# Optimization experiments

Measured on AMD Instinct MI355X. Metric: run time of the kernel, lower is better.

## Reference

```python
import jax, jax.numpy as jnp
import numpy as np

B, S, D, H = 2, 2048, 1024, 16
DK = D // H

def setup_inputs() -> dict:
    key = jax.random.key(0)
    ks = jax.random.split(key, 8)
    inp = {
        "Q": jax.random.normal(ks[0], (B, S, D), dtype=jnp.float32),
        "K": jax.random.normal(ks[1], (B, S, D), dtype=jnp.float32),
        "V": jax.random.normal(ks[2], (B, S, D), dtype=jnp.float32),
        "mask": jax.random.randint(ks[3], (B, 1, S, S), 0, 2, dtype=jnp.int32),
        # nn.Linear weights, shape [out_features, in_features], no bias
        "Wq": jax.random.normal(ks[4], (D, D), dtype=jnp.float32) / np.sqrt(D),
        "Wk": jax.random.normal(ks[5], (D, D), dtype=jnp.float32) / np.sqrt(D),
        "Wv": jax.random.normal(ks[6], (D, D), dtype=jnp.float32) / np.sqrt(D),
        "Wo": jax.random.normal(ks[7], (D, D), dtype=jnp.float32) / np.sqrt(D),
    }
    return inp

def reference(Q, K, V, mask, Wq, Wk, Wv, Wo):
    b, s, d = Q.shape
    # projections: y = x @ W.T (torch nn.Linear convention)
    q = (Q @ Wq.T).reshape(b, s, H, DK).transpose(0, 2, 1, 3)  # [b,h,s,dk]
    k = (K @ Wk.T).reshape(b, -1, H, DK).transpose(0, 2, 1, 3)
    v = (V @ Wv.T).reshape(b, -1, H, DK).transpose(0, 2, 1, 3)
    score = jnp.einsum("bhqd,bhkd->bhqk", q, k) / jnp.sqrt(jnp.float32(DK))
    # faithful to source: masked positions get value 1e-9 BEFORE softmax
    score = jnp.where(mask == 0, jnp.float32(1e-9), score)
    attn = jax.nn.softmax(score, axis=-1)
    # dropout p=0.1 treated as eval-mode identity
    out = jnp.einsum("bhqk,bhkd->bhqd", attn, v)  # [b,h,s,dk]
    out = out.transpose(0, 2, 1, 3).reshape(b, s, d)
    return out @ Wo.T
```

## Files before the change

### kernel.cpp

```cpp
#include <hip/hip_runtime.h>

typedef unsigned short u16;
typedef __attribute__((ext_vector_type(8))) short bf16x8;
typedef __attribute__((ext_vector_type(4))) float f32x4;

constexpr int B_  = 2;
constexpr int S_  = 2048;
constexpr int D_  = 1024;
constexpr int H_  = 16;
constexpr int DK_ = 64;
constexpr int NROW = B_ * S_;
constexpr size_t QSZ = (size_t)B_ * H_ * S_ * DK_;

__device__ __forceinline__ u16 f2bf(float f) {
    union { float f; unsigned u; } c; c.f = f;
    unsigned r = c.u + 0x7fffu + ((c.u >> 16) & 1u);
    return (u16)(r >> 16);
}
__device__ __forceinline__ unsigned pack2(float a, float b) {
    return (unsigned)f2bf(a) | ((unsigned)f2bf(b) << 16);
}

constexpr int GP = 40;

__global__ __launch_bounds__(256, 3)
void qkv_mfma(const float* __restrict__ Xq, const float* __restrict__ Xk,
              const float* __restrict__ Xv,
              const float* __restrict__ Wq, const float* __restrict__ Wk,
              const float* __restrict__ Wv,
              u16* __restrict__ Yq, u16* __restrict__ Yk, u16* __restrict__ Yv)
{
    __shared__ u16 As[128][GP];
    __shared__ u16 Bs[128][GP];

    const int z = blockIdx.z;
    const float* X = (z == 0) ? Xq : (z == 1) ? Xk : Xv;
    const float* W = (z == 0) ? Wq : (z == 1) ? Wk : Wv;
    u16*         Y = (z == 0) ? Yq : (z == 1) ? Yk : Yv;
    const float osc = (z == 0) ? 0.125f : 1.0f;

    const int tid  = threadIdx.x;
    const int lane = tid & 63;
    const int w    = tid >> 6;
    const int quad = lane >> 4;
    const int lq   = lane & 15;
    const int wm   = (w & 1) << 6;
    const int wn   = (w >> 1) << 6;

    const int m0 = blockIdx.x << 7;
    const int n0 = blockIdx.y << 7;

    const int srow = tid >> 1;
    const int skh  = (tid & 1) << 4;

    const float* xrow = X + (size_t)(m0 + srow) * D_ + skh;
    const float* wrow = W + (size_t)(n0 + srow) * D_ + skh;

    f32x4 acc[4][4];
#pragma unroll
    for (int i = 0; i < 4; ++i)
#pragma unroll
        for (int j = 0; j < 4; ++j) acc[i][j] = (f32x4){0.f, 0.f, 0.f, 0.f};

    float4 xa[4], wa[4];
#pragma unroll
    for (int u = 0; u < 4; ++u) {
        xa[u] = *(const float4*)(xrow + (u << 2));
        wa[u] = *(const float4*)(wrow + (u << 2));
    }

    for (int it = 0; it < D_ / 32; ++it) {
        __syncthreads();
        {
            uint4 px, pw;
            px.x = pack2(xa[0].x, xa[0].y); px.y = pack2(xa[0].z, xa[0].w);
            px.z = pack2(xa[1].x, xa[1].y); px.w = pack2(xa[1].z, xa[1].w);
            *(uint4*)&As[srow][skh] = px;
            px.x = pack2(xa[2].x, xa[2].y); px.y = pack2(xa[2].z, xa[2].w);
            px.z = pack2(xa[3].x, xa[3].y); px.w = pack2(xa[3].z, xa[3].w);
            *(uint4*)&As[srow][skh + 8] = px;
            pw.x = pack2(wa[0].x, wa[0].y); pw.y = pack2(wa[0].z, wa[0].w);
            pw.z = pack2(wa[1].x, wa[1].y); pw.w = pack2(wa[1].z, wa[1].w);
            *(uint4*)&Bs[srow][skh] = pw;
            pw.x = pack2(wa[2].x, wa[2].y); pw.y = pack2(wa[2].z, wa[2].w);
            pw.z = pack2(wa[3].x, wa[3].y); pw.w = pack2(wa[3].z, wa[3].w);
            *(uint4*)&Bs[srow][skh + 8] = pw;
        }
        __syncthreads();

        if (it + 1 < D_ / 32) {
            const int kk = (it + 1) << 5;
#pragma unroll
            for (int u = 0; u < 4; ++u) {
                xa[u] = *(const float4*)(xrow + kk + (u << 2));
                wa[u] = *(const float4*)(wrow + kk + (u << 2));
            }
        }

        bf16x8 af[4], bf[4];
#pragma unroll
        for (int t = 0; t < 4; ++t) {
            af[t] = *(const bf16x8*)&As[wm + (t << 4) + lq][quad << 3];
            bf[t] = *(const bf16x8*)&Bs[wn + (t << 4) + lq][quad << 3];
        }
#pragma unroll
        for (int i = 0; i < 4; ++i)
#pragma unroll
            for (int j = 0; j < 4; ++j)
                acc[i][j] = __builtin_amdgcn_mfma_f32_16x16x32_bf16(
                    af[i], bf[j], acc[i][j], 0, 0, 0);
    }

#pragma unroll
    for (int i = 0; i < 4; ++i)
#pragma unroll
        for (int j = 0; j < 4; ++j)
#pragma unroll
            for (int r = 0; r < 4; ++r) {
                const int grow = m0 + wm + (i << 4) + (quad << 2) + r;
                const int of   = n0 + wn + (j << 4) + lq;
                const int b = grow >> 11, s = grow & (S_ - 1);
                const int h = of >> 6,    dk = of & 63;
                Y[(((size_t)(b * H_ + h)) * S_ + s) * DK_ + dk] =
                    f2bf(acc[i][j][r] * osc);
            }
}

__global__ __launch_bounds__(256, 2)
void outproj_mfma(const u16* __restrict__ X, const float* __restrict__ W,
                  float* __restrict__ Y)
{
    __shared__ u16 As[64][GP];
    __shared__ u16 Bs[128][GP];

    const int tid  = threadIdx.x;
    const int lane = tid & 63;
    const int w    = tid >> 6;
    const int quad = lane >> 4;
    const int lq   = lane & 15;
    const int wn   = w << 5;

    const int m0 = blockIdx.x << 6;
    const int n0 = blockIdx.y << 7;

    const int ar = tid >> 2;
    const int ac = (tid & 3) << 3;
    const int br = tid >> 1;
    const int bc = (tid & 1) << 4;

    const u16*   xrow = X + (size_t)(m0 + ar) * D_ + ac;
    const float* wrow = W + (size_t)(n0 + br) * D_ + bc;

    f32x4 acc[4][2];
#pragma unroll
    for (int i = 0; i < 4; ++i)
#pragma unroll
        for (int j = 0; j < 2; ++j) acc[i][j] = (f32x4){0.f, 0.f, 0.f, 0.f};

    uint4 xa; float4 wa[4];
    xa = *(const uint4*)(xrow);
#pragma unroll
    for (int u = 0; u < 4; ++u) wa[u] = *(const float4*)(wrow + (u << 2));

    for (int it = 0; it < D_ / 32; ++it) {
        __syncthreads();
        {
            *(uint4*)&As[ar][ac] = xa;
            uint4 pw;
            pw.x = pack2(wa[0].x, wa[0].y); pw.y = pack2(wa[0].z, wa[0].w);
            pw.z = pack2(wa[1].x, wa[1].y); pw.w = pack2(wa[1].z, wa[1].w);
            *(uint4*)&Bs[br][bc] = pw;
            pw.x = pack2(wa[2].x, wa[2].y); pw.y = pack2(wa[2].z, wa[2].w);
            pw.z = pack2(wa[3].x, wa[3].y); pw.w = pack2(wa[3].z, wa[3].w);
            *(uint4*)&Bs[br][bc + 8] = pw;
        }
        __syncthreads();

        if (it + 1 < D_ / 32) {
            const int kk = (it + 1) << 5;
            xa = *(const uint4*)(xrow + kk);
#pragma unroll
            for (int u = 0; u < 4; ++u)
                wa[u] = *(const float4*)(wrow + kk + (u << 2));
        }

        bf16x8 af[4], bf[2];
#pragma unroll
        for (int t = 0; t < 4; ++t)
            af[t] = *(const bf16x8*)&As[(t << 4) + lq][quad << 3];
#pragma unroll
        for (int j = 0; j < 2; ++j)
            bf[j] = *(const bf16x8*)&Bs[wn + (j << 4) + lq][quad << 3];
#pragma unroll
        for (int i = 0; i < 4; ++i)
#pragma unroll
            for (int j = 0; j < 2; ++j)
                acc[i][j] = __builtin_amdgcn_mfma_f32_16x16x32_bf16(
                    af[i], bf[j], acc[i][j], 0, 0, 0);
    }

#pragma unroll
    for (int i = 0; i < 4; ++i)
#pragma unroll
        for (int j = 0; j < 2; ++j)
#pragma unroll
            for (int r = 0; r < 4; ++r) {
                const int grow = m0 + (i << 4) + (quad << 2) + r;
                const int gcol = n0 + wn + (j << 4) + lq;
                Y[(size_t)grow * D_ + gcol] = acc[i][j][r];
            }
}

constexpr int AP = 72;

__global__ __launch_bounds__(256, 2)
void attn_mfma4(const u16* __restrict__ qb, const u16* __restrict__ kb,
                const u16* __restrict__ vb, const int* __restrict__ mask,
                u16* __restrict__ ctx)
{
    __shared__ u16 Qs[128][AP];
    __shared__ u16 Ks[64][AP];
    __shared__ u16 Vt[64][AP];
    __shared__ u16 Ps[128][AP];

    const int tid  = threadIdx.x;
    const int lane = tid & 63;
    const int w    = tid >> 6;
    const int quad = lane >> 4;
    const int lq   = lane & 15;
    const int w32  = w << 5;

    const int q0 = blockIdx.x << 7;
    const int h  = blockIdx.y;
    const int b  = blockIdx.z;

    const u16* qbh = qb + (((size_t)b * H_ + h) * S_ + q0) * DK_;
    const u16* kbh = kb + ((size_t)b * H_ + h) * S_ * DK_;
    const u16* vbh = vb + ((size_t)b * H_ + h) * S_ * DK_;
    const int* mbh = mask + (size_t)b * S_ * S_;

    {
        const int r = tid >> 1, c = (tid & 1) << 5;
#pragma unroll
        for (int u = 0; u < 4; ++u)
            *(uint4*)&Qs[r][c + (u << 3)] =
                *(const uint4*)&qbh[(size_t)r * DK_ + c + (u << 3)];
    }
    __syncthreads();
    bf16x8 aQ[2][2];
#pragma unroll
    for (int i = 0; i < 2; ++i) {
        aQ[i][0] = *(const bf16x8*)&Qs[w32 + (i << 4) + lq][quad << 3];
        aQ[i][1] = *(const bf16x8*)&Qs[w32 + (i << 4) + lq][32 + (quad << 3)];
    }

    f32x4 O[2][4];
    float lsum[2][4];
#pragma unroll
    for (int i = 0; i < 2; ++i)
#pragma unroll
        for (int t = 0; t < 4; ++t) O[i][t] = (f32x4){0.f, 0.f, 0.f, 0.f};
#pragma unroll
    for (int i = 0; i < 2; ++i)
#pragma unroll
        for (int r = 0; r < 4; ++r) lsum[i][r] = 0.f;

    const int ksr = tid >> 2, ksc = (tid & 3) << 4;
    const int vkey = lane, vsc = w << 4;
    const int vpc  = ((vkey & 15) << 2) | (vkey >> 4);

    uint4 kr0, kr1; ushort4 vr[4];
    {
        kr0 = *(const uint4*)&kbh[(size_t)ksr * DK_ + ksc];
        kr1 = *(const uint4*)&kbh[(size_t)ksr * DK_ + ksc + 8];
#pragma unroll
        for (int u = 0; u < 4; ++u)
            vr[u] = *(const ushort4*)&vbh[(size_t)vkey * DK_ + vsc + (u << 2)];
    }

    const int qrow0 = q0 + w32 + (quad << 2);

    for (int k0 = 0; k0 < S_; k0 += 64) {
        int mreg[2][4][4];
#pragma unroll
        for (int i = 0; i < 2; ++i)
#pragma unroll
            for (int r = 0; r < 4; ++r)
#pragma unroll
                for (int t = 0; t < 4; ++t)
                    mreg[i][r][t] =
                        mbh[(size_t)(qrow0 + (i << 4) + r) * S_ + k0 + (t << 4) + lq];

        __syncthreads();
        {
            *(uint4*)&Ks[ksr][ksc]     = kr0;
            *(uint4*)&Ks[ksr][ksc + 8] = kr1;
            const u16 vv[16] = {
                vr[0].x, vr[0].y, vr[0].z, vr[0].w,
                vr[1].x, vr[1].y, vr[1].z, vr[1].w,
                vr[2].x, vr[2].y, vr[2].z, vr[2].w,
                vr[3].x, vr[3].y, vr[3].z, vr[3].w };
#pragma unroll
            for (int i = 0; i < 16; ++i)
                Vt[vsc + i][vpc] = vv[i];
        }
        __syncthreads();

        if (k0 + 64 < S_) {
            const size_t kb0 = (size_t)(k0 + 64 + ksr) * DK_ + ksc;
            kr0 = *(const uint4*)&kbh[kb0];
            kr1 = *(const uint4*)&kbh[kb0 + 8];
            const size_t vb0 = (size_t)(k0 + 64 + vkey) * DK_ + vsc;
#pragma unroll
            for (int u = 0; u < 4; ++u)
                vr[u] = *(const ushort4*)&vbh[vb0 + (u << 2)];
        }

        f32x4 st[2][4];
#pragma unroll
        for (int t = 0; t < 4; ++t) {
            const bf16x8 b0 = *(const bf16x8*)&Ks[(t << 4) + lq][quad << 3];
            const bf16x8 b1 = *(const bf16x8*)&Ks[(t << 4) + lq][32 + (quad << 3)];
#pragma unroll
            for (int i = 0; i < 2; ++i) {
                f32x4 c = {0.f, 0.f, 0.f, 0.f};
                c = __builtin_amdgcn_mfma_f32_16x16x32_bf16(aQ[i][0], b0, c, 0, 0, 0);
                c = __builtin_amdgcn_mfma_f32_16x16x32_bf16(aQ[i][1], b1, c, 0, 0, 0);
                st[i][t] = c;
            }
        }

#pragma unroll
        for (int i = 0; i < 2; ++i)
#pragma unroll
            for (int r = 0; r < 4; ++r) {
                float p0 = __expf(st[i][0][r]);
                float p1 = __expf(st[i][1][r]);
                float p2 = __expf(st[i][2][r]);
                float p3 = __expf(st[i][3][r]);
                p0 = (mreg[i][r][0] == 0) ? 1.0f : p0;
                p1 = (mreg[i][r][1] == 0) ? 1.0f : p1;
                p2 = (mreg[i][r][2] == 0) ? 1.0f : p2;
                p3 = (mreg[i][r][3] == 0) ? 1.0f : p3;
                lsum[i][r] += (p0 + p1) + (p2 + p3);
                ushort4 pk;
                pk.x = f2bf(p0); pk.y = f2bf(p1);
                pk.z = f2bf(p2); pk.w = f2bf(p3);
                *(ushort4*)&Ps[w32 + (i << 4) + (quad << 2) + r][lq << 2] = pk;
            }

        bf16x8 aP[2][2];
#pragma unroll
        for (int i = 0; i < 2; ++i) {
            aP[i][0] = *(const bf16x8*)&Ps[w32 + (i << 4) + lq][quad << 3];
            aP[i][1] = *(const bf16x8*)&Ps[w32 + (i << 4) + lq][32 + (quad << 3)];
        }
#pragma unroll
        for (int t = 0; t < 4; ++t) {
            const bf16x8 b0 = *(const bf16x8*)&Vt[(t << 4) + lq][quad << 3];
            const bf16x8 b1 = *(const bf16x8*)&Vt[(t << 4) + lq][32 + (quad << 3)];
#pragma unroll
            for (int i = 0; i < 2; ++i) {
                O[i][t] = __builtin_amdgcn_mfma_f32_16x16x32_bf16(aP[i][0], b0, O[i][t], 0, 0, 0);
                O[i][t] = __builtin_amdgcn_mfma_f32_16x16x32_bf16(aP[i][1], b1, O[i][t], 0, 0, 0);
            }
        }
    }

#pragma unroll
    for (int i = 0; i < 2; ++i)
#pragma unroll
        for (int r = 0; r < 4; ++r) {
#pragma unroll
            for (int off = 1; off < 16; off <<= 1)
                lsum[i][r] += __shfl_xor(lsum[i][r], off);
            lsum[i][r] = 1.0f / lsum[i][r];
        }

#pragma unroll
    for (int i = 0; i < 2; ++i)
#pragma unroll
        for (int t = 0; t < 4; ++t)
#pragma unroll
            for (int r = 0; r < 4; ++r) {
                const int row = qrow0 + (i << 4) + r;
                ctx[((size_t)b * S_ + row) * D_ + (h << 6) + (t << 4) + lq] =
                    f2bf(O[i][t][r] * lsum[i][r]);
            }
}

extern "C" void kernel_launch(void* const* d_in, const int* in_sizes, int n_in,
                              void* d_out, int out_size, void* d_ws, size_t ws_size,
                              hipStream_t stream)
{
    const float* Q    = (const float*)d_in[0];
    const float* K    = (const float*)d_in[1];
    const float* V    = (const float*)d_in[2];
    const int*   mask = (const int*)d_in[3];
    const float* Wq   = (const float*)d_in[4];
    const float* Wk   = (const float*)d_in[5];
    const float* Wv   = (const float*)d_in[6];
    const float* Wo   = (const float*)d_in[7];
    float* out = (float*)d_out;

    u16* qw = (u16*)d_ws;
    u16* kw = qw + QSZ;
    u16* vw = qw + 2 * QSZ;
    u16* cx = qw + 3 * QSZ;

    const dim3 blk(256);

    hipLaunchKernelGGL(qkv_mfma, dim3(NROW / 128, D_ / 128, 3), blk, 0, stream,
                       Q, K, V, Wq, Wk, Wv, qw, kw, vw);
    hipLaunchKernelGGL(attn_mfma4, dim3(S_ / 128, H_, B_), blk, 0, stream,
                       qw, kw, vw, mask, cx);
    hipLaunchKernelGGL(outproj_mfma, dim3(NROW / 64, D_ / 128), blk, 0, stream,
                       cx, Wo, out);
}
```

Before: 308.0 us.

## Pre-convert inputs to bf16 and use direct global-to-LDS loads in GEMMs

Adds a conversion kernel that turns all fp32 activations and weights into bf16 workspace buffers once. The QKV and output projection GEMMs then load bf16 tiles straight into LDS with global_load_lds, replacing register staging and in-loop packing. The output GEMM tile also grows to 128x128. This costs an extra kernel launch plus a full fp32 read and bf16 write of every input. The new unpadded LDS layout may cause bank conflicts, and the loop loses its register prefetch overlap.

```diff
diff --git a/kernel.cpp b/kernel.cpp
--- a/kernel.cpp
+++ b/kernel.cpp
@@ -10,7 +10,9 @@
 constexpr int H_  = 16;
 constexpr int DK_ = 64;
 constexpr int NROW = B_ * S_;
-constexpr size_t QSZ = (size_t)B_ * H_ * S_ * DK_;
+constexpr size_t QSZ  = (size_t)B_ * H_ * S_ * DK_;
+constexpr size_t XBSZ = (size_t)NROW * D_;
+constexpr size_t WBSZ = (size_t)D_ * D_;
 
 __device__ __forceinline__ u16 f2bf(float f) {
     union { float f; unsigned u; } c; c.f = f;
@@ -21,22 +23,63 @@
     return (unsigned)f2bf(a) | ((unsigned)f2bf(b) << 16);
 }
 
-constexpr int GP = 40;
+__device__ __forceinline__ void gl_lds16(const u16* g, u16* l) {
+    __builtin_amdgcn_global_load_lds(
+        (const __attribute__((address_space(1))) void*)g,
+        (__attribute__((address_space(3))) void*)l, 16, 0, 0);
+}
+
+__global__ __launch_bounds__(256)
+void cvt7(const float* __restrict__ s0, const float* __restrict__ s1,
+          const float* __restrict__ s2, const float* __restrict__ s3,
+          const float* __restrict__ s4, const float* __restrict__ s5,
+          const float* __restrict__ s6,
+          u16* __restrict__ d0, u16* __restrict__ d1, u16* __restrict__ d2,
+          u16* __restrict__ d3, u16* __restrict__ d4, u16* __restrict__ d5,
+          u16* __restrict__ d6)
+{
+    constexpr size_t XT = 3 * XBSZ;
+    constexpr int NCHUNK = (int)((3 * XBSZ + 4 * WBSZ) / 2048);
+
+    for (int c = blockIdx.x; c < NCHUNK; c += gridDim.x) {
+        const size_t base = (size_t)c * 2048;
+        const float* s; u16* d; size_t off;
+        if (base < XT) {
+            const int a = (int)(base >> 22);
+            off = base & (XBSZ - 1);
+            s = (a == 0) ? s0 : (a == 1) ? s1 : s2;
+            d = (a == 0) ? d0 : (a == 1) ? d1 : d2;
+        } else {
+            const size_t r = base - XT;
+            const int a = (int)(r >> 20);
+            off = r & (WBSZ - 1);
+            s = (a == 0) ? s3 : (a == 1) ? s4 : (a == 2) ? s5 : s6;
+            d = (a == 0) ? d3 : (a == 1) ? d4 : (a == 2) ? d5 : d6;
+        }
+        const size_t e = off + (size_t)threadIdx.x * 8;
+        const float4 x0 = *(const float4*)(s + e);
+        const float4 x1 = *(const float4*)(s + e + 4);
+        uint4 p;
+        p.x = pack2(x0.x, x0.y); p.y = pack2(x0.z, x0.w);
+        p.z = pack2(x1.x, x1.y); p.w = pack2(x1.z, x1.w);
+        *(uint4*)(d + e) = p;
+    }
+}
 
 __global__ __launch_bounds__(256, 3)
-void qkv_mfma(const float* __restrict__ Xq, const float* __restrict__ Xk,
-              const float* __restrict__ Xv,
-              const float* __restrict__ Wq, const float* __restrict__ Wk,
-              const float* __restrict__ Wv,
+void qkv_gemm(const u16* __restrict__ Xq, const u16* __restrict__ Xk,
+              const u16* __restrict__ Xv,
+              const u16* __restrict__ Wq, const u16* __restrict__ Wk,
+              const u16* __restrict__ Wv,
               u16* __restrict__ Yq, u16* __restrict__ Yk, u16* __restrict__ Yv)
 {
-    __shared__ u16 As[128][GP];
-    __shared__ u16 Bs[128][GP];
+    __shared__ u16 As[128 * 32];
+    __shared__ u16 Bs[128 * 32];
 
     const int z = blockIdx.z;
-    const float* X = (z == 0) ? Xq : (z == 1) ? Xk : Xv;
-    const float* W = (z == 0) ? Wq : (z == 1) ? Wk : Wv;
-    u16*         Y = (z == 0) ? Yq : (z == 1) ? Yk : Yv;
+    const u16* X = (z == 0) ? Xq : (z == 1) ? Xk : Xv;
+    const u16* W = (z == 0) ? Wq : (z == 1) ? Wk : Wv;
+    u16*       Y = (z == 0) ? Yq : (z == 1) ? Yk : Yv;
     const float osc = (z == 0) ? 0.125f : 1.0f;
 
     const int tid  = threadIdx.x;
@@ -50,11 +93,17 @@
     const int m0 = blockIdx.x << 7;
     const int n0 = blockIdx.y << 7;
 
-    const int srow = tid >> 1;
-    const int skh  = (tid & 1) << 4;
-
-    const float* xrow = X + (size_t)(m0 + srow) * D_ + skh;
-    const float* wrow = W + (size_t)(n0 + srow) * D_ + skh;
+    const int srow = tid >> 2;
+    const int scol = (tid & 3) << 3;
+    const u16* ga0 = X + (size_t)(m0 + srow) * D_ + scol;
+    const u16* ga1 = ga0 + (size_t)64 * D_;
+    const u16* gb0 = W + (size_t)(n0 + srow) * D_ + scol;
+    const u16* gb1 = gb0 + (size_t)64 * D_;
+
+    u16* la0 = As + (size_t)w * 512;
+    u16* la1 = As + 2048 + (size_t)w * 512;
+    u16* lb0 = Bs + (size_t)w * 512;
+    u16* lb1 = Bs + 2048 + (size_t)w * 512;
 
     f32x4 acc[4][4];
 #pragma unroll
@@ -62,46 +111,19 @@
 #pragma unroll
         for (int j = 0; j < 4; ++j) acc[i][j] = (f32x4){0.f, 0.f, 0.f, 0.f};
 
-    float4 xa[4], wa[4];
-#pragma unroll
-    for (int u = 0; u < 4; ++u) {
-        xa[u] = *(const float4*)(xrow + (u << 2));
-        wa[u] = *(const float4*)(wrow + (u << 2));
-    }
-
-    for (int it = 0; it < D_ / 32; ++it) {
-        __syncthreads();
-        {
-            uint4 px, pw;
-            px.x = pack2(xa[0].x, xa[0].y); px.y = pack2(xa[0].z, xa[0].w);
-            px.z = pack2(xa[1].x, xa[1].y); px.w = pack2(xa[1].z, xa[1].w);
-            *(uint4*)&As[srow][skh] = px;
-            px.x = pack2(xa[2].x, xa[2].y); px.y = pack2(xa[2].z, xa[2].w);
-            px.z = pack2(xa[3].x, xa[3].y); px.w = pack2(xa[3].z, xa[3].w);
-            *(uint4*)&As[srow][skh + 8] = px;
-            pw.x = pack2(wa[0].x, wa[0].y); pw.y = pack2(wa[0].z, wa[0].w);
-            pw.z = pack2(wa[1].x, wa[1].y); pw.w = pack2(wa[1].z, wa[1].w);
-            *(uint4*)&Bs[srow][skh] = pw;
-            pw.x = pack2(wa[2].x, wa[2].y); pw.y = pack2(wa[2].z, wa[2].w);
-            pw.z = pack2(wa[3].x, wa[3].y); pw.w = pack2(wa[3].z, wa[3].w);
-            *(uint4*)&Bs[srow][skh + 8] = pw;
-        }
-        __syncthreads();
-
-        if (it + 1 < D_ / 32) {
-            const int kk = (it + 1) << 5;
-#pragma unroll
-            for (int u = 0; u < 4; ++u) {
-                xa[u] = *(const float4*)(xrow + kk + (u << 2));
-                wa[u] = *(const float4*)(wrow + kk + (u << 2));
-            }
-        }
+    for (int kt = 0; kt < D_; kt += 32) {
+        __syncthreads();
+        gl_lds16(ga0 + kt, la0);
+        gl_lds16(ga1 + kt, la1);
+        gl_lds16(gb0 + kt, lb0);
+        gl_lds16(gb1 + kt, lb1);
+        __syncthreads();
 
         bf16x8 af[4], bf[4];
 #pragma unroll
         for (int t = 0; t < 4; ++t) {
-            af[t] = *(const bf16x8*)&As[wm + (t << 4) + lq][quad << 3];
-            bf[t] = *(const bf16x8*)&Bs[wn + (t << 4) + lq][quad << 3];
+            af[t] = *(const bf16x8*)&As[(size_t)(wm + (t << 4) + lq) * 32 + (quad << 3)];
+            bf[t] = *(const bf16x8*)&Bs[(size_t)(wn + (t << 4) + lq) * 32 + (quad << 3)];
         }
 #pragma unroll
         for (int i = 0; i < 4; ++i)
@@ -126,75 +148,60 @@
             }
 }
 
-__global__ __launch_bounds__(256, 2)
-void outproj_mfma(const u16* __restrict__ X, const float* __restrict__ W,
-                  float* __restrict__ Y)
+__global__ __launch_bounds__(256, 3)
+void out_gemm(const u16* __restrict__ X, const u16* __restrict__ W,
+              float* __restrict__ Y)
 {
-    __shared__ u16 As[64][GP];
-    __shared__ u16 Bs[128][GP];
+    __shared__ u16 As[128 * 32];
+    __shared__ u16 Bs[128 * 32];
 
     const int tid  = threadIdx.x;
     const int lane = tid & 63;
     const int w    = tid >> 6;
     const int quad = lane >> 4;
     const int lq   = lane & 15;
-    const int wn   = w << 5;
-
-    const int m0 = blockIdx.x << 6;
+    const int wm   = (w & 1) << 6;
+    const int wn   = (w >> 1) << 6;
+
+    const int m0 = blockIdx.x << 7;
     const int n0 = blockIdx.y << 7;
 
-    const int ar = tid >> 2;
-    const int ac = (tid & 3) << 3;
-    const int br = tid >> 1;
-    const int bc = (tid & 1) << 4;
-
-    const u16*   xrow = X + (size_t)(m0 + ar) * D_ + ac;
-    const float* wrow = W + (size_t)(n0 + br) * D_ + bc;
-
-    f32x4 acc[4][2];
+    const int srow = tid >> 2;
+    const int scol = (tid & 3) << 3;
+    const u16* ga0 = X + (size_t)(m0 + srow) * D_ + scol;
+    const u16* ga1 = ga0 + (size_t)64 * D_;
+    const u16* gb0 = W + (size_t)(n0 + srow) * D_ + scol;
+    const u16* gb1 = gb0 + (size_t)64 * D_;
+
+    u16* la0 = As + (size_t)w * 512;
+    u16* la1 = As + 2048 + (size_t)w * 512;
+    u16* lb0 = Bs + (size_t)w * 512;
+    u16* lb1 = Bs + 2048 + (size_t)w * 512;
+
+    f32x4 acc[4][4];
 #pragma unroll
     for (int i = 0; i < 4; ++i)
 #pragma unroll
-        for (int j = 0; j < 2; ++j) acc[i][j] = (f32x4){0.f, 0.f, 0.f, 0.f};
-
-    uint4 xa; float4 wa[4];
-    xa = *(const uint4*)(xrow);
-#pragma unroll
-    for (int u = 0; u < 4; ++u) wa[u] = *(const float4*)(wrow + (u << 2));
-
-    for (int it = 0; it < D_ / 32; ++it) {
-        __syncthreads();
-        {
-            *(uint4*)&As[ar][ac] = xa;
-            uint4 pw;
-            pw.x = pack2(wa[0].x, wa[0].y); pw.y = pack2(wa[0].z, wa[0].w);
-            pw.z = pack2(wa[1].x, wa[1].y); pw.w = pack2(wa[1].z, wa[1].w);
-            *(uint4*)&Bs[br][bc] = pw;
-            pw.x = pack2(wa[2].x, wa[2].y); pw.y = pack2(wa[2].z, wa[2].w);
-            pw.z = pack2(wa[3].x, wa[3].y); pw.w = pack2(wa[3].z, wa[3].w);
-            *(uint4*)&Bs[br][bc + 8] = pw;
-        }
-        __syncthreads();
-
-        if (it + 1 < D_ / 32) {
-            const int kk = (it + 1) << 5;
-            xa = *(const uint4*)(xrow + kk);
-#pragma unroll
-            for (int u = 0; u < 4; ++u)
-                wa[u] = *(const float4*)(wrow + kk + (u << 2));
-        }
-
-        bf16x8 af[4], bf[2];
-#pragma unroll
-        for (int t = 0; t < 4; ++t)
-            af[t] = *(const bf16x8*)&As[(t << 4) + lq][quad << 3];
-#pragma unroll
-        for (int j = 0; j < 2; ++j)
-            bf[j] = *(const bf16x8*)&Bs[wn + (j << 4) + lq][quad << 3];
+        for (int j = 0; j < 4; ++j) acc[i][j] = (f32x4){0.f, 0.f, 0.f, 0.f};
+
+    for (int kt = 0; kt < D_; kt += 32) {
+        __syncthreads();
+        gl_lds16(ga0 + kt, la0);
+        gl_lds16(ga1 + kt, la1);
+        gl_lds16(gb0 + kt, lb0);
+        gl_lds16(gb1 + kt, lb1);
+        __syncthreads();
+
+        bf16x8 af[4], bf[4];
+#pragma unroll
+        for (int t = 0; t < 4; ++t) {
+            af[t] = *(const bf16x8*)&As[(size_t)(wm + (t << 4) + lq) * 32 + (quad << 3)];
+            bf[t] = *(const bf16x8*)&Bs[(size_t)(wn + (t << 4) + lq) * 32 + (quad << 3)];
+        }
 #pragma unroll
         for (int i = 0; i < 4; ++i)
 #pragma unroll
-            for (int j = 0; j < 2; ++j)
+            for (int j = 0; j < 4; ++j)
                 acc[i][j] = __builtin_amdgcn_mfma_f32_16x16x32_bf16(
                     af[i], bf[j], acc[i][j], 0, 0, 0);
     }
@@ -202,10 +209,10 @@
 #pragma unroll
     for (int i = 0; i < 4; ++i)
 #pragma unroll
-        for (int j = 0; j < 2; ++j)
+        for (int j = 0; j < 4; ++j)
 #pragma unroll
             for (int r = 0; r < 4; ++r) {
-                const int grow = m0 + (i << 4) + (quad << 2) + r;
+                const int grow = m0 + wm + (i << 4) + (quad << 2) + r;
                 const int gcol = n0 + wn + (j << 4) + lq;
                 Y[(size_t)grow * D_ + gcol] = acc[i][j][r];
             }
@@ -403,17 +410,27 @@
     const float* Wo   = (const float*)d_in[7];
     float* out = (float*)d_out;
 
-    u16* qw = (u16*)d_ws;
-    u16* kw = qw + QSZ;
-    u16* vw = qw + 2 * QSZ;
-    u16* cx = qw + 3 * QSZ;
+    u16* xqb = (u16*)d_ws;
+    u16* xkb = xqb + XBSZ;
+    u16* xvb = xqb + 2 * XBSZ;
+    u16* wqb = xqb + 3 * XBSZ;
+    u16* wkb = wqb + WBSZ;
+    u16* wvb = wqb + 2 * WBSZ;
+    u16* wob = wqb + 3 * WBSZ;
+    u16* qw  = wqb + 4 * WBSZ;
+    u16* kw  = qw + QSZ;
+    u16* vw  = qw + 2 * QSZ;
+    u16* cx  = xqb;
 
     const dim3 blk(256);
 
-    hipLaunchKernelGGL(qkv_mfma, dim3(NROW / 128, D_ / 128, 3), blk, 0, stream,
-                       Q, K, V, Wq, Wk, Wv, qw, kw, vw);
+    hipLaunchKernelGGL(cvt7, dim3(2048), blk, 0, stream,
+                       Q, K, V, Wq, Wk, Wv, Wo,
+                       xqb, xkb, xvb, wqb, wkb, wvb, wob);
+    hipLaunchKernelGGL(qkv_gemm, dim3(NROW / 128, D_ / 128, 3), blk, 0, stream,
+                       xqb, xkb, xvb, wqb, wkb, wvb, qw, kw, vw);
     hipLaunchKernelGGL(attn_mfma4, dim3(S_ / 128, H_, B_), blk, 0, stream,
                        qw, kw, vw, mask, cx);
-    hipLaunchKernelGGL(outproj_mfma, dim3(NROW / 64, D_ / 128), blk, 0, stream,
-                       cx, Wo, out);
-}
+    hipLaunchKernelGGL(out_gemm, dim3(NROW / 128, D_ / 128), blk, 0, stream,
+                       cx, wob, out);
+}
```

Result: faster. 257.0 us (-16.6%).
